# Optimization experiments

Measured on AMD Instinct MI355X. Metric: run time of the kernel, lower is better.

Reference implementation:

```python
import jax, jax.numpy as jnp
import numpy as np

HIDDEN = 1024
HEADS = 16
HEAD_DIM = HIDDEN // HEADS
POS_DIM = 128
B, S = 2, 2048
ROPE_BASE = 10000.0


def setup_inputs() -> dict:
    key = jax.random.key(0)
    ks = jax.random.split(key, 8)
    sd = 1.0 / np.sqrt(HIDDEN)
    return {
        "x":   jax.random.normal(ks[0], (B, S, HIDDEN), dtype=jnp.float32),
        "W_q": jax.random.normal(ks[1], (HIDDEN, HIDDEN), dtype=jnp.float32) * sd,
        "W_k": jax.random.normal(ks[2], (HIDDEN, HIDDEN), dtype=jnp.float32) * sd,
        "W_v": jax.random.normal(ks[3], (HIDDEN, HIDDEN), dtype=jnp.float32) * sd,
        "W_o": jax.random.normal(ks[4], (HIDDEN, HIDDEN), dtype=jnp.float32) * sd,
        "repo_W1": jax.random.normal(ks[5], (HIDDEN, POS_DIM), dtype=jnp.float32) * sd,
        "repo_b1": jnp.zeros((POS_DIM,), dtype=jnp.float32),
        "repo_W2": jax.random.normal(ks[6], (POS_DIM, 1), dtype=jnp.float32) * (1.0 / np.sqrt(POS_DIM)),
        "repo_b2": jnp.zeros((1,), dtype=jnp.float32),
    }


def _repo_positions(x, W1, b1, W2, b2):
    # 2-layer MLP -> scalar per token; softplus + cumsum gives monotone learned positions
    h = jax.nn.gelu(jnp.einsum("bsd,dp->bsp", x, W1) + b1)
    raw = (jnp.einsum("bsp,po->bso", h, W2) + b2)[..., 0]      # (B, S)
    return jnp.cumsum(jax.nn.softplus(raw), axis=1)             # (B, S)


def _apply_rope(q, k, positions):
    # q, k: (B, S, H, Dh); positions: (B, S) continuous
    half = HEAD_DIM // 2
    inv_freq = 1.0 / (ROPE_BASE ** (jnp.arange(0, HEAD_DIM, 2, dtype=jnp.float32) / HEAD_DIM))
    angles = positions[:, :, None] * inv_freq                   # (B, S, half)
    cos = jnp.cos(angles)[:, :, None, :]                        # (B, S, 1, half)
    sin = jnp.sin(angles)[:, :, None, :]

    def rot(t):
        t1, t2 = t[..., :half], t[..., half:]
        return jnp.concatenate([t1 * cos - t2 * sin, t1 * sin + t2 * cos], axis=-1)

    return rot(q), rot(k)


def reference(x, W_q, W_k, W_v, W_o, repo_W1, repo_b1, repo_W2, repo_b2):
    scale = 1.0 / np.sqrt(HEAD_DIM)
    q = jnp.einsum("bsd,de->bse", x, W_q).reshape(B, S, HEADS, HEAD_DIM)
    k = jnp.einsum("bsd,de->bse", x, W_k).reshape(B, S, HEADS, HEAD_DIM)
    v = jnp.einsum("bsd,de->bse", x, W_v).reshape(B, S, HEADS, HEAD_DIM)

    positions = _repo_positions(x, repo_W1, repo_b1, repo_W2, repo_b2)
    q, k = _apply_rope(q, k, positions)

    # explicit O(S^2) attention, matching the torch module
    scores = jnp.einsum("bqhd,bkhd->bhqk", q, k) * scale        # (B, H, S, S)
    attn = jax.nn.softmax(scores, axis=-1)
    out = jnp.einsum("bhqk,bkhd->bqhd", attn, v)                # (B, S, H, Dh)
    out = out.reshape(B, S, HIDDEN)
    return jnp.einsum("bsd,de->bse", out, W_o)
```

## Files before the change

### kernel.cpp

```cpp
#include <hip/hip_runtime.h>
#include <hip/hip_bf16.h>
#include <math.h>

#define HIDDEN 1024
#define HEADS 16
#define HEAD_DIM 64
#define POS_DIM 128
#define BATCH 2
#define SEQ 2048
#define TOKENS (BATCH * SEQ)

typedef _Float16 f16;
typedef __attribute__((ext_vector_type(8))) _Float16 f16x8;
typedef __attribute__((ext_vector_type(4))) _Float16 f16x4;
typedef __attribute__((ext_vector_type(4))) float f32x4;

__device__ __forceinline__ void glds16(const f16* g, f16* l) {
    __builtin_amdgcn_global_load_lds((const __attribute__((address_space(1))) unsigned int*)g,
                                     (__attribute__((address_space(3))) unsigned int*)l, 16, 0, 0);
}

__global__ __launch_bounds__(256) void cast_all_kernel(const float* __restrict__ x,
                                                       const float* __restrict__ W0,
                                                       const float* __restrict__ W1,
                                                       const float* __restrict__ W2,
                                                       const float* __restrict__ W3,
                                                       const float* __restrict__ rW1,
                                                       f16* __restrict__ x16,
                                                       f16* __restrict__ Wt,
                                                       f16* __restrict__ Wh,
                                                       f16* __restrict__ Wl) {
    __shared__ float ts[32][33];
    const int bid = blockIdx.x;
    const int t = threadIdx.x;
    if (bid < 2048) {
        const int i = (bid * 256 + t) * 8;
        const float4 u = *(const float4*)(x + i);
        const float4 v = *(const float4*)(x + i + 4);
        f16x8 r = {(f16)u.x, (f16)u.y, (f16)u.z, (f16)u.w,
                   (f16)v.x, (f16)v.y, (f16)v.z, (f16)v.w};
        *(f16x8*)(x16 + i) = r;
        return;
    }
    if (bid < 6144) {
        const int local = bid - 2048;
        const int z = local >> 10;
        const int by = (local & 1023) >> 5, bx = local & 31;
        const float* W = (z == 0) ? W0 : (z == 1) ? W1 : (z == 2) ? W2 : W3;
        f16* dst = Wt + (size_t)z * HIDDEN * HIDDEN;
        const int k0 = by * 32, n0 = bx * 32;
        {
            const int r = t >> 3, c4 = (t & 7) * 4;
            const float4 u = *(const float4*)(W + (size_t)(k0 + r) * HIDDEN + n0 + c4);
            ts[r][c4 + 0] = u.x; ts[r][c4 + 1] = u.y; ts[r][c4 + 2] = u.z; ts[r][c4 + 3] = u.w;
        }
        __syncthreads();
        {
            const int r = t >> 3, c4 = (t & 7) * 4;
            f16* o = dst + (size_t)(n0 + r) * HIDDEN + k0 + c4;
            o[0] = (f16)ts[c4 + 0][r]; o[1] = (f16)ts[c4 + 1][r];
            o[2] = (f16)ts[c4 + 2][r]; o[3] = (f16)ts[c4 + 3][r];
        }
        return;
    }
    {
        const int local = bid - 6144;
        const int k0 = (local >> 2) * 32, p0 = (local & 3) * 32;
        {
            const int r = t >> 3, c4 = (t & 7) * 4;
            const float4 u = *(const float4*)(rW1 + (size_t)(k0 + r) * POS_DIM + p0 + c4);
            ts[r][c4 + 0] = u.x; ts[r][c4 + 1] = u.y; ts[r][c4 + 2] = u.z; ts[r][c4 + 3] = u.w;
        }
        __syncthreads();
        {
            const int r = t >> 3, c4 = (t & 7) * 4;
            f16* oh = Wh + (size_t)(p0 + r) * HIDDEN + k0 + c4;
            f16* ol = Wl + (size_t)(p0 + r) * HIDDEN + k0 + c4;
#pragma unroll
            for (int u = 0; u < 4; ++u) {
                const float v = ts[c4 + u][r];
                const f16 hi = (f16)v;
                oh[u] = hi;
                ol[u] = (f16)(v - (float)hi);
            }
        }
    }
}

__global__ __launch_bounds__(256, 3) void gemm_gll(const f16* __restrict__ A,
                                                   const f16* __restrict__ Bt,
                                                   f16* __restrict__ Cb,
                                                   float* __restrict__ Cf,
                                                   int N, int f16out) {
    __shared__ __align__(16) f16 As[128 * 64];
    __shared__ __align__(16) f16 Bs[128 * 64];
    const int tid = threadIdx.x;
    const int w = tid >> 6, lane = tid & 63;
    const int g = lane >> 4, c = lane & 15;
    const int m0 = blockIdx.y * 128, n0 = blockIdx.x * 128;
    const int wm = (w & 1) * 64, wn = (w >> 1) * 64;

    const int lrow = lane >> 3;
    const int lseg = (lane & 7) ^ lrow;
    const f16* gA = A + (size_t)(m0 + w * 32 + lrow) * 1024 + lseg * 8;
    const f16* gB = Bt + (size_t)(n0 + w * 32 + lrow) * 1024 + lseg * 8;
    f16* lA = &As[(w * 32) * 64];
    f16* lB = &Bs[(w * 32) * 64];

    f32x4 acc[4][4];
    const f32x4 z = {0.f, 0.f, 0.f, 0.f};
#pragma unroll
    for (int i = 0; i < 4; ++i)
#pragma unroll
        for (int j = 0; j < 4; ++j) acc[i][j] = z;

    const int rsw = c & 7;
    for (int k0 = 0; k0 < 1024; k0 += 64) {
        __syncthreads();
#pragma unroll
        for (int p = 0; p < 4; ++p) {
            glds16(gA + (size_t)p * 8 * 1024 + k0, lA + p * 8 * 64);
            glds16(gB + (size_t)p * 8 * 1024 + k0, lB + p * 8 * 64);
        }
        __syncthreads();
#pragma unroll
        for (int s = 0; s < 2; ++s) {
            f16x8 af[4], bf[4];
#pragma unroll
            for (int i = 0; i < 4; ++i)
                af[i] = *(const f16x8*)&As[(wm + i * 16 + c) * 64 + (((s * 4 + g) ^ rsw) * 8)];
#pragma unroll
            for (int j = 0; j < 4; ++j)
                bf[j] = *(const f16x8*)&Bs[(wn + j * 16 + c) * 64 + (((s * 4 + g) ^ rsw) * 8)];
#pragma unroll
            for (int i = 0; i < 4; ++i)
#pragma unroll
                for (int j = 0; j < 4; ++j)
                    acc[i][j] = __builtin_amdgcn_mfma_f32_16x16x32_f16(bf[j], af[i], acc[i][j], 0, 0, 0);
        }
    }
#pragma unroll
    for (int i = 0; i < 4; ++i)
#pragma unroll
        for (int j = 0; j < 4; ++j) {
            const size_t off = (size_t)(m0 + wm + i * 16 + c) * N + n0 + wn + j * 16 + 4 * g;
            if (f16out) {
                f16x4 v = {(f16)acc[i][j][0], (f16)acc[i][j][1],
                           (f16)acc[i][j][2], (f16)acc[i][j][3]};
                *(f16x4*)(Cb + off) = v;
            } else {
                *(f32x4*)(Cf + off) = acc[i][j];
            }
        }
}

__global__ __launch_bounds__(256, 4) void gemm_gll64(const f16* __restrict__ A,
                                                     const f16* __restrict__ Bt,
                                                     float* __restrict__ Cf,
                                                     int N) {
    __shared__ __align__(16) f16 As[64 * 64];
    __shared__ __align__(16) f16 Bs[128 * 64];
    const int tid = threadIdx.x;
    const int w = tid >> 6, lane = tid & 63;
    const int g = lane >> 4, c = lane & 15;
    const int m0 = blockIdx.y * 64, n0 = blockIdx.x * 128;
    const int wm = (w & 1) * 32, wn = (w >> 1) * 64;

    const int lrow = lane >> 3;
    const int lseg = (lane & 7) ^ lrow;
    const f16* gA = A + (size_t)(m0 + w * 16 + lrow) * 1024 + lseg * 8;
    const f16* gB = Bt + (size_t)(n0 + w * 32 + lrow) * 1024 + lseg * 8;
    f16* lA = &As[(w * 16) * 64];
    f16* lB = &Bs[(w * 32) * 64];

    f32x4 acc[2][4];
    const f32x4 z = {0.f, 0.f, 0.f, 0.f};
#pragma unroll
    for (int i = 0; i < 2; ++i)
#pragma unroll
        for (int j = 0; j < 4; ++j) acc[i][j] = z;

    const int rsw = c & 7;
    for (int k0 = 0; k0 < 1024; k0 += 64) {
        __syncthreads();
#pragma unroll
        for (int p = 0; p < 2; ++p)
            glds16(gA + (size_t)p * 8 * 1024 + k0, lA + p * 8 * 64);
#pragma unroll
        for (int p = 0; p < 4; ++p)
            glds16(gB + (size_t)p * 8 * 1024 + k0, lB + p * 8 * 64);
        __syncthreads();
#pragma unroll
        for (int s = 0; s < 2; ++s) {
            f16x8 af[2], bf[4];
#pragma unroll
            for (int i = 0; i < 2; ++i)
                af[i] = *(const f16x8*)&As[(wm + i * 16 + c) * 64 + (((s * 4 + g) ^ rsw) * 8)];
#pragma unroll
            for (int j = 0; j < 4; ++j)
                bf[j] = *(const f16x8*)&Bs[(wn + j * 16 + c) * 64 + (((s * 4 + g) ^ rsw) * 8)];
#pragma unroll
            for (int i = 0; i < 2; ++i)
#pragma unroll
                for (int j = 0; j < 4; ++j)
                    acc[i][j] = __builtin_amdgcn_mfma_f32_16x16x32_f16(bf[j], af[i], acc[i][j], 0, 0, 0);
        }
    }
#pragma unroll
    for (int i = 0; i < 2; ++i)
#pragma unroll
        for (int j = 0; j < 4; ++j) {
            const size_t off = (size_t)(m0 + wm + i * 16 + c) * N + n0 + wn + j * 16 + 4 * g;
            *(f32x4*)(Cf + off) = acc[i][j];
        }
}

__device__ __forceinline__ float gelu_tanh(float x) {
    const float kA = 0.7978845608028654f;
    return 0.5f * x * (1.0f + tanhf(kA * (x + 0.044715f * x * x * x)));
}

__global__ __launch_bounds__(256, 2) void repo_mfma(const float* __restrict__ x,
                                                    const f16* __restrict__ w1h,
                                                    const f16* __restrict__ w1l,
                                                    const float* __restrict__ b1,
                                                    const float* __restrict__ W2,
                                                    const float* __restrict__ b2,
                                                    float* __restrict__ raw) {
    __shared__ __align__(16) f16 Ash[64 * 32], Asl[64 * 32];
    __shared__ __align__(16) f16 Bsh[128 * 32], Bsl[128 * 32];
    __shared__ float red[4][64];
    const int tid = threadIdx.x;
    const int w = tid >> 6, lane = tid & 63;
    const int g = lane >> 4, c = lane & 15;
    const int m0 = blockIdx.x * 64;

    const int arow = tid >> 2, aseg = tid & 3;
    const int aslot = (aseg ^ ((arow ^ (arow >> 2)) & 3)) << 3;
    const float* gA = x + (size_t)(m0 + arow) * 1024 + aseg * 8;
    const f16* gBh0 = w1h + (size_t)arow * 1024 + aseg * 8;
    const f16* gBh1 = w1h + (size_t)(arow + 64) * 1024 + aseg * 8;
    const f16* gBl0 = w1l + (size_t)arow * 1024 + aseg * 8;
    const f16* gBl1 = w1l + (size_t)(arow + 64) * 1024 + aseg * 8;
    f16* sAh = &Ash[arow * 32 + aslot];
    f16* sAl = &Asl[arow * 32 + aslot];
    f16* sBh0 = &Bsh[arow * 32 + aslot];
    f16* sBh1 = &Bsh[(arow + 64) * 32 + aslot];
    f16* sBl0 = &Bsl[arow * 32 + aslot];
    f16* sBl1 = &Bsl[(arow + 64) * 32 + aslot];

    const int foff = ((g ^ ((c ^ (c >> 2)) & 3)) << 3);

    f32x4 acc[4][2];
    const f32x4 z = {0.f, 0.f, 0.f, 0.f};
#pragma unroll
    for (int i = 0; i < 4; ++i) { acc[i][0] = z; acc[i][1] = z; }

    float4 pa0 = *(const float4*)gA;
    float4 pa1 = *(const float4*)(gA + 4);
    f16x8 pbh0 = *(const f16x8*)gBh0, pbh1 = *(const f16x8*)gBh1;
    f16x8 pbl0 = *(const f16x8*)gBl0, pbl1 = *(const f16x8*)gBl1;

    for (int k0 = 0; k0 < 1024; k0 += 32) {
        __syncthreads();
        {
            const float av[8] = {pa0.x, pa0.y, pa0.z, pa0.w, pa1.x, pa1.y, pa1.z, pa1.w};
            f16x8 ah, al;
#pragma unroll
            for (int u = 0; u < 8; ++u) {
                const f16 hi = (f16)av[u];
                ah[u] = hi;
                al[u] = (f16)(av[u] - (float)hi);
            }
            *(f16x8*)sAh = ah; *(f16x8*)sAl = al;
            *(f16x8*)sBh0 = pbh0; *(f16x8*)sBh1 = pbh1;
            *(f16x8*)sBl0 = pbl0; *(f16x8*)sBl1 = pbl1;
        }
        __syncthreads();
        if (k0 + 32 < 1024) {
            pa0 = *(const float4*)(gA + k0 + 32);
            pa1 = *(const float4*)(gA + k0 + 36);
            pbh0 = *(const f16x8*)(gBh0 + k0 + 32);
            pbh1 = *(const f16x8*)(gBh1 + k0 + 32);
            pbl0 = *(const f16x8*)(gBl0 + k0 + 32);
            pbl1 = *(const f16x8*)(gBl1 + k0 + 32);
        }
        f16x8 ah[4], al[4], bh[2], bl[2];
#pragma unroll
        for (int i = 0; i < 4; ++i) {
            ah[i] = *(const f16x8*)&Ash[(i * 16 + c) * 32 + foff];
            al[i] = *(const f16x8*)&Asl[(i * 16 + c) * 32 + foff];
        }
#pragma unroll
        for (int j = 0; j < 2; ++j) {
            bh[j] = *(const f16x8*)&Bsh[(w * 32 + j * 16 + c) * 32 + foff];
            bl[j] = *(const f16x8*)&Bsl[(w * 32 + j * 16 + c) * 32 + foff];
        }
#pragma unroll
        for (int i = 0; i < 4; ++i)
#pragma unroll
            for (int j = 0; j < 2; ++j) {
                acc[i][j] = __builtin_amdgcn_mfma_f32_16x16x32_f16(ah[i], bh[j], acc[i][j], 0, 0, 0);
                acc[i][j] = __builtin_amdgcn_mfma_f32_16x16x32_f16(ah[i], bl[j], acc[i][j], 0, 0, 0);
                acc[i][j] = __builtin_amdgcn_mfma_f32_16x16x32_f16(al[i], bh[j], acc[i][j], 0, 0, 0);
            }
    }
    float b1v[2], w2v[2];
#pragma unroll
    for (int j = 0; j < 2; ++j) {
        const int col = w * 32 + j * 16 + c;
        b1v[j] = b1[col];
        w2v[j] = W2[col];
    }
    float part[4][4];
#pragma unroll
    for (int i = 0; i < 4; ++i)
#pragma unroll
        for (int r = 0; r < 4; ++r) {
            float s = 0.f;
#pragma unroll
            for (int j = 0; j < 2; ++j)
                s += gelu_tanh(acc[i][j][r] + b1v[j]) * w2v[j];
            s += __shfl_xor(s, 1, 64);
            s += __shfl_xor(s, 2, 64);
            s += __shfl_xor(s, 4, 64);
            s += __shfl_xor(s, 8, 64);
            part[i][r] = s;
        }
    if (c == 0)
#pragma unroll
        for (int i = 0; i < 4; ++i)
#pragma unroll
            for (int r = 0; r < 4; ++r)
                red[w][i * 16 + 4 * g + r] = part[i][r];
    __syncthreads();
    if (tid < 64)
        raw[m0 + tid] = red[0][tid] + red[1][tid] + red[2][tid] + red[3][tid] + b2[0];
}

__device__ __forceinline__ double softplus_d(double x) {
    return (x > 0.0) ? x + log1p(exp(-x)) : log1p(exp(x));
}

__global__ __launch_bounds__(256) void repo_cumsum_kernel(const float* __restrict__ raw,
                                                          float* __restrict__ pos) {
    __shared__ double bufA[256];
    __shared__ double bufB[256];
    const int b = blockIdx.x;
    const int t = threadIdx.x;
    const float* r = raw + (size_t)b * SEQ;

    double loc[8];
    double sum = 0.0;
#pragma unroll
    for (int i = 0; i < 8; ++i) {
        sum += softplus_d((double)r[t * 8 + i]);
        loc[i] = sum;
    }
    bufA[t] = sum;
    __syncthreads();

    double* src = bufA;
    double* dst = bufB;
    for (int off = 1; off < 256; off <<= 1) {
        double v = src[t];
        if (t >= off) v += src[t - off];
        dst[t] = v;
        __syncthreads();
        double* tmp = src; src = dst; dst = tmp;
    }
    const double excl = src[t] - sum;
#pragma unroll
    for (int i = 0; i < 8; ++i)
        pos[(size_t)b * SEQ + t * 8 + i] = (float)(excl + loc[i]);
}

__global__ __launch_bounds__(256) void sctab_kernel(const float* __restrict__ pos,
                                                    float* __restrict__ costab,
                                                    float* __restrict__ sintab) {
    const int idx = blockIdx.x * 256 + threadIdx.x;
    const int tok = idx >> 5, i = idx & 31;
    const double ang = (double)pos[tok] * exp(-(double)i * 0.28782313662425574);
    double sa, ca;
    sincos(ang, &sa, &ca);
    costab[idx] = (float)ca;
    sintab[idx] = (float)sa;
}

__global__ __launch_bounds__(256) void packkv_kernel(f16* __restrict__ qkv,
                                                     const float* __restrict__ costab,
                                                     const float* __restrict__ sintab,
                                                     f16* __restrict__ kfo,
                                                     f16* __restrict__ vfo) {
    __shared__ __align__(16) f16 kds[64][72];
    __shared__ __align__(16) f16 vds[64][72];
    const int t = threadIdx.x;
    const int s0 = blockIdx.x * 64;
    const int h = blockIdx.y, b = blockIdx.z;
    const int key = t >> 2, part = t & 3;
    const int tok = b * SEQ + s0 + key;
    {
        float cs[8], sn[8];
        *(float4*)cs       = *(const float4*)(costab + tok * 32 + part * 8);
        *(float4*)(cs + 4) = *(const float4*)(costab + tok * 32 + part * 8 + 4);
        *(float4*)sn       = *(const float4*)(sintab + tok * 32 + part * 8);
        *(float4*)(sn + 4) = *(const float4*)(sintab + tok * 32 + part * 8 + 4);
        f16* qrow = qkv + (size_t)tok * 3072 + h * HEAD_DIM;
        {
            f16x8 lo = *(const f16x8*)(qrow + part * 8);
            f16x8 hi = *(const f16x8*)(qrow + part * 8 + 32);
#pragma unroll
            for (int u = 0; u < 8; ++u) {
                const float l = (float)lo[u], hh = (float)hi[u];
                lo[u] = (f16)(l * cs[u] - hh * sn[u]);
                hi[u] = (f16)(l * sn[u] + hh * cs[u]);
            }
            *(f16x8*)(qrow + part * 8) = lo;
            *(f16x8*)(qrow + part * 8 + 32) = hi;
        }
        const f16* krow = qrow + 1024;
        {
            f16x8 lo = *(const f16x8*)(krow + part * 8);
            f16x8 hi = *(const f16x8*)(krow + part * 8 + 32);
#pragma unroll
            for (int u = 0; u < 8; ++u) {
                const float l = (float)lo[u], hh = (float)hi[u];
                kds[key][part * 8 + u]      = (f16)(l * cs[u] - hh * sn[u]);
                kds[key][32 + part * 8 + u] = (f16)(l * sn[u] + hh * cs[u]);
            }
        }
        const f16* vrow = qrow + 2048;
        f16x8 v0 = *(const f16x8*)(vrow + part * 16);
        f16x8 v1 = *(const f16x8*)(vrow + part * 16 + 8);
#pragma unroll
        for (int u = 0; u < 8; ++u) {
            vds[part * 16 + u][key] = v0[u];
            vds[part * 16 + 8 + u][key] = v1[u];
        }
    }
    __syncthreads();
    const size_t cb = ((size_t)((b * HEADS + h) * 32) + blockIdx.x) * 4096;
#pragma unroll
    for (int p = 0; p < 2; ++p) {
        const int idx = p * 256 + t;
        const int frag = idx >> 6, lane = idx & 63;
        const int jn = frag >> 1, half = frag & 1, g = lane >> 4, c = lane & 15;
        *(f16x8*)(kfo + cb + frag * 512 + lane * 8) =
            *(const f16x8*)(&kds[jn * 16 + c][half * 32 + g * 8]);
    }
#pragma unroll
    for (int p = 0; p < 4; ++p) {
        const int idx = p * 256 + t;
        const int frag = idx >> 6, lane = idx & 63;
        const int jd = frag >> 2, jn = frag & 3, g = lane >> 4, c = lane & 15;
        *(f16x4*)(vfo + cb + frag * 256 + lane * 4) =
            *(const f16x4*)(&vds[jd * 16 + c][jn * 16 + 4 * g]);
    }
}

__global__ __launch_bounds__(256, 2) void attn_f16(const f16* __restrict__ qkv,
                                                   const f16* __restrict__ kfr,
                                                   const f16* __restrict__ vfr,
                                                   f16* __restrict__ aof0) {
    __shared__ __align__(16) f16 kls[4096];
    __shared__ __align__(16) f16 vls[4096];
    __shared__ __align__(16) f16 ot[4][32][72];
    const int tid = threadIdx.x;
    const int w = tid >> 6, lane = tid & 63;
    const int g = lane >> 4, c = lane & 15;

    const int wid = blockIdx.x;
    const int xcd = wid & 7, slot = wid >> 3;
    const int combo = xcd * 4 + (slot >> 4);
    const int xblk = slot & 15;
    const int h = combo & 15;
    const int b = combo >> 4;

    const int bh = b * HEADS + h;
    const int row0 = xblk * 128 + w * 32;

    const f16* qb = qkv + (size_t)(b * SEQ + row0) * 3072 + h * HEAD_DIM + g * 8;
    const f16* kfb = kfr + (size_t)bh * 32 * 4096 + w * 1024 + lane * 8;
    const f16* vfb = vfr + (size_t)bh * 32 * 4096 + w * 1024 + lane * 8;
    f16* kd = kls + w * 1024 + lane * 8;
    f16* vd = vls + w * 1024 + lane * 8;

    f16x8 qf[2][2];
#pragma unroll
    for (int i = 0; i < 2; ++i) {
        qf[i][0] = *(const f16x8*)(qb + (size_t)(i * 16 + c) * 3072);
        qf[i][1] = *(const f16x8*)(qb + (size_t)(i * 16 + c) * 3072 + 32);
    }
    const f32x4 z = {0.f, 0.f, 0.f, 0.f};
    f32x4 acc[4][2];
#pragma unroll
    for (int jd = 0; jd < 4; ++jd) { acc[jd][0] = z; acc[jd][1] = z; }
    float dloc[2] = {0.f, 0.f};

    const float SC = 0.125f * 1.4426950408889634f;

    f16x8 kr0 = *(const f16x8*)(kfb);
    f16x8 kr1 = *(const f16x8*)(kfb + 512);
    f16x8 vr0 = *(const f16x8*)(vfb);
    f16x8 vr1 = *(const f16x8*)(vfb + 512);

    for (int cc = 0; cc < 32; ++cc) {
        __syncthreads();
        *(f16x8*)kd         = kr0;
        *(f16x8*)(kd + 512) = kr1;
        *(f16x8*)vd         = vr0;
        *(f16x8*)(vd + 512) = vr1;
        __syncthreads();
        if (cc + 1 < 32) {
            const f16* kg = kfb + (size_t)(cc + 1) * 4096;
            const f16* vg = vfb + (size_t)(cc + 1) * 4096;
            kr0 = *(const f16x8*)(kg);
            kr1 = *(const f16x8*)(kg + 512);
            vr0 = *(const f16x8*)(vg);
            vr1 = *(const f16x8*)(vg + 512);
        }

        f16x8 kf[8];
        f16x4 vf[16];
#pragma unroll
        for (int f = 0; f < 8; ++f) kf[f] = *(const f16x8*)(kls + lane * 8 + f * 512);
#pragma unroll
        for (int f = 0; f < 16; ++f) vf[f] = *(const f16x4*)(vls + lane * 4 + f * 256);

#pragma unroll
        for (int i = 0; i < 2; ++i) {
            f32x4 s[4];
#pragma unroll
            for (int jn = 0; jn < 4; ++jn) {
                s[jn] = __builtin_amdgcn_mfma_f32_16x16x32_f16(kf[jn * 2], qf[i][0], z, 0, 0, 0);
                s[jn] = __builtin_amdgcn_mfma_f32_16x16x32_f16(kf[jn * 2 + 1], qf[i][1], s[jn], 0, 0, 0);
            }
#pragma unroll
            for (int jn = 0; jn < 4; ++jn) {
                const float e0 = __builtin_amdgcn_exp2f(fmaf(s[jn][0], SC, -8.0f));
                const float e1 = __builtin_amdgcn_exp2f(fmaf(s[jn][1], SC, -8.0f));
                const float e2 = __builtin_amdgcn_exp2f(fmaf(s[jn][2], SC, -8.0f));
                const float e3 = __builtin_amdgcn_exp2f(fmaf(s[jn][3], SC, -8.0f));
                dloc[i] += (e0 + e1) + (e2 + e3);
                f16x4 pf = {(f16)e0, (f16)e1, (f16)e2, (f16)e3};
#pragma unroll
                for (int jd = 0; jd < 4; ++jd)
                    acc[jd][i] = __builtin_amdgcn_mfma_f32_16x16x16f16(vf[jd * 4 + jn], pf, acc[jd][i], 0, 0, 0);
            }
        }
    }

    float inv[2];
#pragma unroll
    for (int i = 0; i < 2; ++i) {
        dloc[i] += __shfl_xor(dloc[i], 16, 64);
        dloc[i] += __shfl_xor(dloc[i], 32, 64);
        inv[i] = 1.0f / dloc[i];
    }

    __syncthreads();
#pragma unroll
    for (int i = 0; i < 2; ++i)
#pragma unroll
        for (int jd = 0; jd < 4; ++jd)
#pragma unroll
            for (int r = 0; r < 4; ++r)
                ot[w][i * 16 + c][jd * 16 + 4 * g + r] = (f16)(acc[jd][i][r] * inv[i]);
    const int tr = lane >> 1, hf = lane & 1;
    f16* aob = aof0 + (size_t)(b * SEQ + row0 + tr) * HIDDEN + h * HEAD_DIM + hf * 32;
#pragma unroll
    for (int q = 0; q < 4; ++q)
        *(f16x8*)(aob + q * 8) = *(const f16x8*)(&ot[w][tr][hf * 32 + q * 8]);
}

extern "C" void kernel_launch(void* const* d_in, const int* in_sizes, int n_in,
                              void* d_out, int out_size, void* d_ws, size_t ws_size,
                              hipStream_t stream) {
    const float* x   = (const float*)d_in[0];
    const float* W_q = (const float*)d_in[1];
    const float* W_k = (const float*)d_in[2];
    const float* W_v = (const float*)d_in[3];
    const float* W_o = (const float*)d_in[4];
    const float* rW1 = (const float*)d_in[5];
    const float* rb1 = (const float*)d_in[6];
    const float* rW2 = (const float*)d_in[7];
    const float* rb2 = (const float*)d_in[8];
    float* out = (float*)d_out;

    const size_t MAT = (size_t)TOKENS * HIDDEN;
    const size_t WSZ = (size_t)HIDDEN * HIDDEN;
    f16* x16  = (f16*)d_ws;
    f16* wqkv = x16 + MAT;
    f16* wot  = wqkv + 3 * WSZ;
    f16* qkv  = wot + WSZ;
    f16* kfr  = qkv + 3 * MAT;
    f16* vfr  = kfr + MAT;
    f16* aof0 = vfr + MAT;
    f16* aof1 = aof0 + MAT;
    f16* w1h  = aof1 + MAT;
    f16* w1l  = w1h + POS_DIM * HIDDEN;
    float* raw    = (float*)(w1l + POS_DIM * HIDDEN);
    float* pos    = raw + TOKENS;
    float* costab = pos + TOKENS;
    float* sintab = costab + TOKENS * 32;

    cast_all_kernel<<<6272, 256, 0, stream>>>(x, W_q, W_k, W_v, W_o, rW1,
                                              x16, wqkv, w1h, w1l);

    gemm_gll<<<dim3(24, 32), 256, 0, stream>>>(x16, wqkv, qkv, nullptr, 3072, 1);

    repo_mfma<<<64, 256, 0, stream>>>(x, w1h, w1l, rb1, rW2, rb2, raw);
    repo_cumsum_kernel<<<BATCH, 256, 0, stream>>>(raw, pos);
    sctab_kernel<<<TOKENS * 32 / 256, 256, 0, stream>>>(pos, costab, sintab);

    packkv_kernel<<<dim3(SEQ / 64, HEADS, BATCH), 256, 0, stream>>>(qkv, costab, sintab, kfr, vfr);

    attn_f16<<<dim3(512), 256, 0, stream>>>(qkv, kfr, vfr, aof0);

    gemm_gll64<<<dim3(8, 64), 256, 0, stream>>>(aof0, wot, out, 1024);
}
```

Measured before the change: 239.8 us.

## Merge QKV GEMM and repo MLP into one launch with shared smem union

Combines the QKV projection GEMM and the repo-position MLP kernel into one grid. The first 64 blocks do the repo MLP and the remaining 768 blocks do QKV GEMM tiles, with shared memory held in a union. This removes a launch and lets the small, long-running repo blocks overlap with the GEMM tiles. In exchange, launch bounds drop from 3 to 2 waves per SIMD for the GEMM path, which may lower its occupancy.

```diff
diff --git a/kernel.cpp b/kernel.cpp
--- a/kernel.cpp
+++ b/kernel.cpp
@@ -87,71 +87,194 @@
     }
 }
 
-__global__ __launch_bounds__(256, 3) void gemm_gll(const f16* __restrict__ A,
-                                                   const f16* __restrict__ Bt,
-                                                   f16* __restrict__ Cb,
-                                                   float* __restrict__ Cf,
-                                                   int N, int f16out) {
-    __shared__ __align__(16) f16 As[128 * 64];
-    __shared__ __align__(16) f16 Bs[128 * 64];
+__device__ __forceinline__ float gelu_tanh(float x) {
+    const float kA = 0.7978845608028654f;
+    return 0.5f * x * (1.0f + tanhf(kA * (x + 0.044715f * x * x * x)));
+}
+
+union SmemPool {
+    struct { f16 As[128 * 64]; f16 Bs[128 * 64]; } g;
+    struct { f16 Ash[64 * 32]; f16 Asl[64 * 32];
+             f16 Bsh[128 * 32]; f16 Bsl[128 * 32]; float red[4][64]; } r;
+};
+
+__global__ __launch_bounds__(256, 2) void gemm_repo_kernel(
+        const f16* __restrict__ A, const f16* __restrict__ Bt, f16* __restrict__ Cb,
+        const float* __restrict__ x,
+        const f16* __restrict__ w1h, const f16* __restrict__ w1l,
+        const float* __restrict__ b1, const float* __restrict__ W2,
+        const float* __restrict__ b2, float* __restrict__ raw) {
+    __shared__ __align__(16) SmemPool sp;
+    const int bid = blockIdx.x;
     const int tid = threadIdx.x;
     const int w = tid >> 6, lane = tid & 63;
     const int g = lane >> 4, c = lane & 15;
-    const int m0 = blockIdx.y * 128, n0 = blockIdx.x * 128;
-    const int wm = (w & 1) * 64, wn = (w >> 1) * 64;
-
-    const int lrow = lane >> 3;
-    const int lseg = (lane & 7) ^ lrow;
-    const f16* gA = A + (size_t)(m0 + w * 32 + lrow) * 1024 + lseg * 8;
-    const f16* gB = Bt + (size_t)(n0 + w * 32 + lrow) * 1024 + lseg * 8;
-    f16* lA = &As[(w * 32) * 64];
-    f16* lB = &Bs[(w * 32) * 64];
-
-    f32x4 acc[4][4];
-    const f32x4 z = {0.f, 0.f, 0.f, 0.f};
-#pragma unroll
-    for (int i = 0; i < 4; ++i)
-#pragma unroll
-        for (int j = 0; j < 4; ++j) acc[i][j] = z;
-
-    const int rsw = c & 7;
-    for (int k0 = 0; k0 < 1024; k0 += 64) {
-        __syncthreads();
-#pragma unroll
-        for (int p = 0; p < 4; ++p) {
-            glds16(gA + (size_t)p * 8 * 1024 + k0, lA + p * 8 * 64);
-            glds16(gB + (size_t)p * 8 * 1024 + k0, lB + p * 8 * 64);
-        }
-        __syncthreads();
-#pragma unroll
-        for (int s = 0; s < 2; ++s) {
-            f16x8 af[4], bf[4];
+
+    if (bid < 64) {
+        f16* Ash = sp.r.Ash; f16* Asl = sp.r.Asl;
+        f16* Bsh = sp.r.Bsh; f16* Bsl = sp.r.Bsl;
+        float (*red)[64] = sp.r.red;
+        const int m0 = bid * 64;
+
+        const int arow = tid >> 2, aseg = tid & 3;
+        const int aslot = (aseg ^ ((arow ^ (arow >> 2)) & 3)) << 3;
+        const float* gA = x + (size_t)(m0 + arow) * 1024 + aseg * 8;
+        const f16* gBh0 = w1h + (size_t)arow * 1024 + aseg * 8;
+        const f16* gBh1 = w1h + (size_t)(arow + 64) * 1024 + aseg * 8;
+        const f16* gBl0 = w1l + (size_t)arow * 1024 + aseg * 8;
+        const f16* gBl1 = w1l + (size_t)(arow + 64) * 1024 + aseg * 8;
+        f16* sAh = &Ash[arow * 32 + aslot];
+        f16* sAl = &Asl[arow * 32 + aslot];
+        f16* sBh0 = &Bsh[arow * 32 + aslot];
+        f16* sBh1 = &Bsh[(arow + 64) * 32 + aslot];
+        f16* sBl0 = &Bsl[arow * 32 + aslot];
+        f16* sBl1 = &Bsl[(arow + 64) * 32 + aslot];
+
+        const int foff = ((g ^ ((c ^ (c >> 2)) & 3)) << 3);
+
+        f32x4 acc[4][2];
+        const f32x4 z = {0.f, 0.f, 0.f, 0.f};
+#pragma unroll
+        for (int i = 0; i < 4; ++i) { acc[i][0] = z; acc[i][1] = z; }
+
+        float4 pa0 = *(const float4*)gA;
+        float4 pa1 = *(const float4*)(gA + 4);
+        f16x8 pbh0 = *(const f16x8*)gBh0, pbh1 = *(const f16x8*)gBh1;
+        f16x8 pbl0 = *(const f16x8*)gBl0, pbl1 = *(const f16x8*)gBl1;
+
+        for (int k0 = 0; k0 < 1024; k0 += 32) {
+            __syncthreads();
+            {
+                const float av[8] = {pa0.x, pa0.y, pa0.z, pa0.w, pa1.x, pa1.y, pa1.z, pa1.w};
+                f16x8 ah, al;
+#pragma unroll
+                for (int u = 0; u < 8; ++u) {
+                    const f16 hi = (f16)av[u];
+                    ah[u] = hi;
+                    al[u] = (f16)(av[u] - (float)hi);
+                }
+                *(f16x8*)sAh = ah; *(f16x8*)sAl = al;
+                *(f16x8*)sBh0 = pbh0; *(f16x8*)sBh1 = pbh1;
+                *(f16x8*)sBl0 = pbl0; *(f16x8*)sBl1 = pbl1;
+            }
+            __syncthreads();
+            if (k0 + 32 < 1024) {
+                pa0 = *(const float4*)(gA + k0 + 32);
+                pa1 = *(const float4*)(gA + k0 + 36);
+                pbh0 = *(const f16x8*)(gBh0 + k0 + 32);
+                pbh1 = *(const f16x8*)(gBh1 + k0 + 32);
+                pbl0 = *(const f16x8*)(gBl0 + k0 + 32);
+                pbl1 = *(const f16x8*)(gBl1 + k0 + 32);
+            }
+            f16x8 ah[4], al[4], bh[2], bl[2];
+#pragma unroll
+            for (int i = 0; i < 4; ++i) {
+                ah[i] = *(const f16x8*)&Ash[(i * 16 + c) * 32 + foff];
+                al[i] = *(const f16x8*)&Asl[(i * 16 + c) * 32 + foff];
+            }
+#pragma unroll
+            for (int j = 0; j < 2; ++j) {
+                bh[j] = *(const f16x8*)&Bsh[(w * 32 + j * 16 + c) * 32 + foff];
+                bl[j] = *(const f16x8*)&Bsl[(w * 32 + j * 16 + c) * 32 + foff];
+            }
 #pragma unroll
             for (int i = 0; i < 4; ++i)
-                af[i] = *(const f16x8*)&As[(wm + i * 16 + c) * 64 + (((s * 4 + g) ^ rsw) * 8)];
-#pragma unroll
-            for (int j = 0; j < 4; ++j)
-                bf[j] = *(const f16x8*)&Bs[(wn + j * 16 + c) * 64 + (((s * 4 + g) ^ rsw) * 8)];
+#pragma unroll
+                for (int j = 0; j < 2; ++j) {
+                    acc[i][j] = __builtin_amdgcn_mfma_f32_16x16x32_f16(ah[i], bh[j], acc[i][j], 0, 0, 0);
+                    acc[i][j] = __builtin_amdgcn_mfma_f32_16x16x32_f16(ah[i], bl[j], acc[i][j], 0, 0, 0);
+                    acc[i][j] = __builtin_amdgcn_mfma_f32_16x16x32_f16(al[i], bh[j], acc[i][j], 0, 0, 0);
+                }
+        }
+        float b1v[2], w2v[2];
+#pragma unroll
+        for (int j = 0; j < 2; ++j) {
+            const int col = w * 32 + j * 16 + c;
+            b1v[j] = b1[col];
+            w2v[j] = W2[col];
+        }
+        float part[4][4];
+#pragma unroll
+        for (int i = 0; i < 4; ++i)
+#pragma unroll
+            for (int r = 0; r < 4; ++r) {
+                float s = 0.f;
+#pragma unroll
+                for (int j = 0; j < 2; ++j)
+                    s += gelu_tanh(acc[i][j][r] + b1v[j]) * w2v[j];
+                s += __shfl_xor(s, 1, 64);
+                s += __shfl_xor(s, 2, 64);
+                s += __shfl_xor(s, 4, 64);
+                s += __shfl_xor(s, 8, 64);
+                part[i][r] = s;
+            }
+        if (c == 0)
 #pragma unroll
             for (int i = 0; i < 4; ++i)
 #pragma unroll
+                for (int r = 0; r < 4; ++r)
+                    red[w][i * 16 + 4 * g + r] = part[i][r];
+        __syncthreads();
+        if (tid < 64)
+            raw[m0 + tid] = red[0][tid] + red[1][tid] + red[2][tid] + red[3][tid] + b2[0];
+        return;
+    }
+
+    {
+        f16* As = sp.g.As; f16* Bs = sp.g.Bs;
+        const int gid = bid - 64;
+        const int m0 = (gid / 24) * 128, n0 = (gid % 24) * 128;
+        const int wm = (w & 1) * 64, wn = (w >> 1) * 64;
+
+        const int lrow = lane >> 3;
+        const int lseg = (lane & 7) ^ lrow;
+        const f16* gA = A + (size_t)(m0 + w * 32 + lrow) * 1024 + lseg * 8;
+        const f16* gB = Bt + (size_t)(n0 + w * 32 + lrow) * 1024 + lseg * 8;
+        f16* lA = &As[(w * 32) * 64];
+        f16* lB = &Bs[(w * 32) * 64];
+
+        f32x4 acc[4][4];
+        const f32x4 z = {0.f, 0.f, 0.f, 0.f};
+#pragma unroll
+        for (int i = 0; i < 4; ++i)
+#pragma unroll
+            for (int j = 0; j < 4; ++j) acc[i][j] = z;
+
+        const int rsw = c & 7;
+        for (int k0 = 0; k0 < 1024; k0 += 64) {
+            __syncthreads();
+#pragma unroll
+            for (int p = 0; p < 4; ++p) {
+                glds16(gA + (size_t)p * 8 * 1024 + k0, lA + p * 8 * 64);
+                glds16(gB + (size_t)p * 8 * 1024 + k0, lB + p * 8 * 64);
+            }
+            __syncthreads();
+#pragma unroll
+            for (int s = 0; s < 2; ++s) {
+                f16x8 af[4], bf[4];
+#pragma unroll
+                for (int i = 0; i < 4; ++i)
+                    af[i] = *(const f16x8*)&As[(wm + i * 16 + c) * 64 + (((s * 4 + g) ^ rsw) * 8)];
+#pragma unroll
                 for (int j = 0; j < 4; ++j)
-                    acc[i][j] = __builtin_amdgcn_mfma_f32_16x16x32_f16(bf[j], af[i], acc[i][j], 0, 0, 0);
-        }
-    }
-#pragma unroll
-    for (int i = 0; i < 4; ++i)
-#pragma unroll
-        for (int j = 0; j < 4; ++j) {
-            const size_t off = (size_t)(m0 + wm + i * 16 + c) * N + n0 + wn + j * 16 + 4 * g;
-            if (f16out) {
+                    bf[j] = *(const f16x8*)&Bs[(wn + j * 16 + c) * 64 + (((s * 4 + g) ^ rsw) * 8)];
+#pragma unroll
+                for (int i = 0; i < 4; ++i)
+#pragma unroll
+                    for (int j = 0; j < 4; ++j)
+                        acc[i][j] = __builtin_amdgcn_mfma_f32_16x16x32_f16(bf[j], af[i], acc[i][j], 0, 0, 0);
+            }
+        }
+#pragma unroll
+        for (int i = 0; i < 4; ++i)
+#pragma unroll
+            for (int j = 0; j < 4; ++j) {
+                const size_t off = (size_t)(m0 + wm + i * 16 + c) * 3072 + n0 + wn + j * 16 + 4 * g;
                 f16x4 v = {(f16)acc[i][j][0], (f16)acc[i][j][1],
                            (f16)acc[i][j][2], (f16)acc[i][j][3]};
                 *(f16x4*)(Cb + off) = v;
-            } else {
-                *(f32x4*)(Cf + off) = acc[i][j];
-            }
-        }
+            }
+    }
 }
 
 __global__ __launch_bounds__(256, 4) void gemm_gll64(const f16* __restrict__ A,
@@ -213,129 +336,6 @@
             const size_t off = (size_t)(m0 + wm + i * 16 + c) * N + n0 + wn + j * 16 + 4 * g;
             *(f32x4*)(Cf + off) = acc[i][j];
         }
-}
-
-__device__ __forceinline__ float gelu_tanh(float x) {
-    const float kA = 0.7978845608028654f;
-    return 0.5f * x * (1.0f + tanhf(kA * (x + 0.044715f * x * x * x)));
-}
-
-__global__ __launch_bounds__(256, 2) void repo_mfma(const float* __restrict__ x,
-                                                    const f16* __restrict__ w1h,
-                                                    const f16* __restrict__ w1l,
-                                                    const float* __restrict__ b1,
-                                                    const float* __restrict__ W2,
-                                                    const float* __restrict__ b2,
-                                                    float* __restrict__ raw) {
-    __shared__ __align__(16) f16 Ash[64 * 32], Asl[64 * 32];
-    __shared__ __align__(16) f16 Bsh[128 * 32], Bsl[128 * 32];
-    __shared__ float red[4][64];
-    const int tid = threadIdx.x;
-    const int w = tid >> 6, lane = tid & 63;
-    const int g = lane >> 4, c = lane & 15;
-    const int m0 = blockIdx.x * 64;
-
-    const int arow = tid >> 2, aseg = tid & 3;
-    const int aslot = (aseg ^ ((arow ^ (arow >> 2)) & 3)) << 3;
-    const float* gA = x + (size_t)(m0 + arow) * 1024 + aseg * 8;
-    const f16* gBh0 = w1h + (size_t)arow * 1024 + aseg * 8;
-    const f16* gBh1 = w1h + (size_t)(arow + 64) * 1024 + aseg * 8;
-    const f16* gBl0 = w1l + (size_t)arow * 1024 + aseg * 8;
-    const f16* gBl1 = w1l + (size_t)(arow + 64) * 1024 + aseg * 8;
-    f16* sAh = &Ash[arow * 32 + aslot];
-    f16* sAl = &Asl[arow * 32 + aslot];
-    f16* sBh0 = &Bsh[arow * 32 + aslot];
-    f16* sBh1 = &Bsh[(arow + 64) * 32 + aslot];
-    f16* sBl0 = &Bsl[arow * 32 + aslot];
-    f16* sBl1 = &Bsl[(arow + 64) * 32 + aslot];
-
-    const int foff = ((g ^ ((c ^ (c >> 2)) & 3)) << 3);
-
-    f32x4 acc[4][2];
-    const f32x4 z = {0.f, 0.f, 0.f, 0.f};
-#pragma unroll
-    for (int i = 0; i < 4; ++i) { acc[i][0] = z; acc[i][1] = z; }
-
-    float4 pa0 = *(const float4*)gA;
-    float4 pa1 = *(const float4*)(gA + 4);
-    f16x8 pbh0 = *(const f16x8*)gBh0, pbh1 = *(const f16x8*)gBh1;
-    f16x8 pbl0 = *(const f16x8*)gBl0, pbl1 = *(const f16x8*)gBl1;
-
-    for (int k0 = 0; k0 < 1024; k0 += 32) {
-        __syncthreads();
-        {
-            const float av[8] = {pa0.x, pa0.y, pa0.z, pa0.w, pa1.x, pa1.y, pa1.z, pa1.w};
-            f16x8 ah, al;
-#pragma unroll
-            for (int u = 0; u < 8; ++u) {
-                const f16 hi = (f16)av[u];
-                ah[u] = hi;
-                al[u] = (f16)(av[u] - (float)hi);
-            }
-            *(f16x8*)sAh = ah; *(f16x8*)sAl = al;
-            *(f16x8*)sBh0 = pbh0; *(f16x8*)sBh1 = pbh1;
-            *(f16x8*)sBl0 = pbl0; *(f16x8*)sBl1 = pbl1;
-        }
-        __syncthreads();
-        if (k0 + 32 < 1024) {
-            pa0 = *(const float4*)(gA + k0 + 32);
-            pa1 = *(const float4*)(gA + k0 + 36);
-            pbh0 = *(const f16x8*)(gBh0 + k0 + 32);
-            pbh1 = *(const f16x8*)(gBh1 + k0 + 32);
-            pbl0 = *(const f16x8*)(gBl0 + k0 + 32);
-            pbl1 = *(const f16x8*)(gBl1 + k0 + 32);
-        }
-        f16x8 ah[4], al[4], bh[2], bl[2];
-#pragma unroll
-        for (int i = 0; i < 4; ++i) {
-            ah[i] = *(const f16x8*)&Ash[(i * 16 + c) * 32 + foff];
-            al[i] = *(const f16x8*)&Asl[(i * 16 + c) * 32 + foff];
-        }
-#pragma unroll
-        for (int j = 0; j < 2; ++j) {
-            bh[j] = *(const f16x8*)&Bsh[(w * 32 + j * 16 + c) * 32 + foff];
-            bl[j] = *(const f16x8*)&Bsl[(w * 32 + j * 16 + c) * 32 + foff];
-        }
-#pragma unroll
-        for (int i = 0; i < 4; ++i)
-#pragma unroll
-            for (int j = 0; j < 2; ++j) {
-                acc[i][j] = __builtin_amdgcn_mfma_f32_16x16x32_f16(ah[i], bh[j], acc[i][j], 0, 0, 0);
-                acc[i][j] = __builtin_amdgcn_mfma_f32_16x16x32_f16(ah[i], bl[j], acc[i][j], 0, 0, 0);
-                acc[i][j] = __builtin_amdgcn_mfma_f32_16x16x32_f16(al[i], bh[j], acc[i][j], 0, 0, 0);
-            }
-    }
-    float b1v[2], w2v[2];
-#pragma unroll
-    for (int j = 0; j < 2; ++j) {
-        const int col = w * 32 + j * 16 + c;
-        b1v[j] = b1[col];
-        w2v[j] = W2[col];
-    }
-    float part[4][4];
-#pragma unroll
-    for (int i = 0; i < 4; ++i)
-#pragma unroll
-        for (int r = 0; r < 4; ++r) {
-            float s = 0.f;
-#pragma unroll
-            for (int j = 0; j < 2; ++j)
-                s += gelu_tanh(acc[i][j][r] + b1v[j]) * w2v[j];
-            s += __shfl_xor(s, 1, 64);
-            s += __shfl_xor(s, 2, 64);
-            s += __shfl_xor(s, 4, 64);
-            s += __shfl_xor(s, 8, 64);
-            part[i][r] = s;
-        }
-    if (c == 0)
-#pragma unroll
-        for (int i = 0; i < 4; ++i)
-#pragma unroll
-            for (int r = 0; r < 4; ++r)
-                red[w][i * 16 + 4 * g + r] = part[i][r];
-    __syncthreads();
-    if (tid < 64)
-        raw[m0 + tid] = red[0][tid] + red[1][tid] + red[2][tid] + red[3][tid] + b2[0];
 }
 
 __device__ __forceinline__ double softplus_d(double x) {
@@ -607,9 +607,9 @@
     cast_all_kernel<<<6272, 256, 0, stream>>>(x, W_q, W_k, W_v, W_o, rW1,
                                               x16, wqkv, w1h, w1l);
 
-    gemm_gll<<<dim3(24, 32), 256, 0, stream>>>(x16, wqkv, qkv, nullptr, 3072, 1);
-
-    repo_mfma<<<64, 256, 0, stream>>>(x, w1h, w1l, rb1, rW2, rb2, raw);
+    gemm_repo_kernel<<<832, 256, 0, stream>>>(x16, wqkv, qkv,
+                                              x, w1h, w1l, rb1, rW2, rb2, raw);
+
     repo_cumsum_kernel<<<BATCH, 256, 0, stream>>>(raw, pos);
     sctab_kernel<<<TOKENS * 32 / 256, 256, 0, stream>>>(pos, costab, sintab);
 
```

Measured after the change: 219.4 us. 1.09x faster.
